# Optimization experiments

Measured on AMD Instinct MI355X. Metric: run time of the kernel, lower is better.

Reference implementation:

```python
import jax, jax.numpy as jnp
import numpy as np

EMBED_DIM = 768
NUM_HEADS = 12
HEAD_DIM = EMBED_DIM // NUM_HEADS
MEMORY_SIZE = 64
B, T = 8, 1024


def setup_inputs() -> dict:
    key = jax.random.key(0)
    ks = jax.random.split(key, 8)
    s = 0.02
    return {
        "x": jax.random.normal(ks[0], (B, T, EMBED_DIM), dtype=jnp.float32),
        "w_qkv": jax.random.normal(ks[1], (EMBED_DIM, 3 * EMBED_DIM), dtype=jnp.float32) * s,
        "b_qkv": jax.random.normal(ks[2], (3 * EMBED_DIM,), dtype=jnp.float32) * s,
        "w_out": jax.random.normal(ks[3], (EMBED_DIM, EMBED_DIM), dtype=jnp.float32) * s,
        "b_out": jax.random.normal(ks[4], (EMBED_DIM,), dtype=jnp.float32) * s,
        "w_mem": jax.random.normal(ks[5], (EMBED_DIM, EMBED_DIM), dtype=jnp.float32) * s,
        "b_mem": jax.random.normal(ks[6], (EMBED_DIM,), dtype=jnp.float32) * s,
        "memory": jax.random.normal(ks[7], (1, MEMORY_SIZE, EMBED_DIM), dtype=jnp.float32),
    }


def reference(x, w_qkv, b_qkv, w_out, b_out, w_mem, b_mem, memory):
    Bx, Tx, C = x.shape
    H, D = NUM_HEADS, HEAD_DIM
    scale = 1.0 / np.sqrt(D).astype(np.float32)

    # qkv projection -> (3, B, H, T, D)
    qkv = (x @ w_qkv + b_qkv).reshape(Bx, Tx, 3, H, D)
    qkv = jnp.transpose(qkv, (2, 0, 3, 1, 4))
    q, k, v = qkv[0], qkv[1], qkv[2]

    # full (non-causal) local attention over T
    scores = jnp.einsum("bhqd,bhkd->bhqk", q, k) * scale  # (B,H,T,T)
    local_out = jnp.einsum("bhqk,bhkd->bhqd", jax.nn.softmax(scores, axis=-1), v)

    # memory attention: projected memory serves as both K and V
    mem = memory @ w_mem + b_mem                      # (1, M, C)
    mem = jnp.broadcast_to(mem, (Bx, MEMORY_SIZE, C))
    mem_kv = jnp.transpose(mem.reshape(Bx, MEMORY_SIZE, H, D), (0, 2, 1, 3))  # (B,H,M,D)
    mem_scores = jnp.einsum("bhqd,bhmd->bhqm", q, mem_kv) * scale
    mem_out = jnp.einsum("bhqm,bhmd->bhqd", jax.nn.softmax(mem_scores, axis=-1), mem_kv)

    out = (local_out + mem_out).transpose(0, 2, 1, 3).reshape(Bx, Tx, C)
    return out @ w_out + b_out
```

## Files before the change

kernel.cpp:

```cpp
#include <hip/hip_runtime.h>

#define EMBED 768
#define NH 12
#define HD 64
#define MEMN 64
#define BB 8
#define TT 1024
#define ROWS 8192
#define QKV_N 2304
#define QSZ 6291456

typedef short bf16x8_t __attribute__((ext_vector_type(8)));
typedef float f32x4_t __attribute__((ext_vector_type(4)));

__device__ __forceinline__ unsigned short f2b(float f){
    union { float f; unsigned int i; } v; v.f = f;
    unsigned int x = v.i;
    unsigned int r = x + 0x7fffu + ((x >> 16) & 1u);
    return (unsigned short)(r >> 16);
}
__device__ __forceinline__ unsigned short f2b_ru(float f){
    union { float f; unsigned int i; } v; v.f = f;
    return (unsigned short)((v.i + 0x8000u) >> 16);
}

__device__ __forceinline__ void gl16(const unsigned short* g, unsigned short* l){
    __builtin_amdgcn_global_load_lds(
        (const __attribute__((address_space(1))) void*)g,
        (__attribute__((address_space(3))) void*)l,
        16, 0, 0);
}

#define SCHED_FENCE() __builtin_amdgcn_sched_barrier(0)

#define PREP_CVT   3072
#define PREP_TQKV  4800
#define PREP_TOUT  5376
#define PREP_TOTAL 5388

__global__ __launch_bounds__(256) void prep_kernel(
    const float* __restrict__ x,
    const float* __restrict__ w_qkv,
    const float* __restrict__ w_out,
    const float* __restrict__ memory,
    const float* __restrict__ w_mem,
    const float* __restrict__ b_mem,
    unsigned short* __restrict__ xb,
    unsigned short* __restrict__ wqkvT,
    unsigned short* __restrict__ woutT,
    unsigned short* __restrict__ mem_k,
    unsigned short* __restrict__ mem_v)
{
    __shared__ unsigned short pool[5120];
    const int bid = blockIdx.x;
    const int t = threadIdx.x;

    if (bid < PREP_CVT) {
        int i = bid * 2048 + t * 8;
        float4 f0 = *(const float4*)&x[i];
        float4 f1 = *(const float4*)&x[i + 4];
        union { bf16x8_t v; unsigned short s[8]; } u;
        u.s[0] = f2b(f0.x); u.s[1] = f2b(f0.y); u.s[2] = f2b(f0.z); u.s[3] = f2b(f0.w);
        u.s[4] = f2b(f1.x); u.s[5] = f2b(f1.y); u.s[6] = f2b(f1.z); u.s[7] = f2b(f1.w);
        *(bf16x8_t*)&xb[i] = u.v;
    } else if (bid < PREP_TOUT) {
        const float* in; unsigned short* out; int R, C, loc;
        if (bid < PREP_TQKV) { in = w_qkv; out = wqkvT; R = EMBED; C = QKV_N; loc = bid - PREP_CVT; }
        else                 { in = w_out; out = woutT; R = EMBED; C = EMBED; loc = bid - PREP_TQKV; }
        int nbc = C / 32;
        int bc = (loc % nbc) * 32, br = (loc / nbc) * 32;
        unsigned short (*tile)[33] = (unsigned short(*)[33])pool;
        int lr = t >> 5, lc = t & 31;
        for (int i = 0; i < 4; i++) {
            int r = lr + i * 8;
            tile[r][lc] = f2b(in[(size_t)(br + r) * C + bc + lc]);
        }
        __syncthreads();
        for (int i = 0; i < 4; i++) {
            int r = lr + i * 8;
            out[(size_t)(bc + r) * R + br + lc] = tile[lc][r];
        }
    } else {
        unsigned short (*As)[40] = (unsigned short(*)[40])pool;
        unsigned short (*Bs)[40] = (unsigned short(*)[40])(pool + 2560);
        int wave = t >> 6, lane = t & 63;
        int ln = lane & 15, lq = lane >> 4;
        int bn = (bid - PREP_TOUT) * 64;
        const int K = EMBED, N = EMBED;

        f32x4_t acc[4];
        for (int i = 0; i < 4; i++) acc[i] = (f32x4_t)(0.f);
        int sm = t >> 2, sk = (t & 3) * 8;
        int bk = t >> 3, bn8 = (t & 7) * 8;

        for (int k0 = 0; k0 < K; k0 += 32) {
            __syncthreads();
            {
                float4 f0 = *(const float4*)&memory[(size_t)sm * K + k0 + sk];
                float4 f1 = *(const float4*)&memory[(size_t)sm * K + k0 + sk + 4];
                unsigned short* ap = &As[sm][sk];
                ap[0] = f2b(f0.x); ap[1] = f2b(f0.y); ap[2] = f2b(f0.z); ap[3] = f2b(f0.w);
                ap[4] = f2b(f1.x); ap[5] = f2b(f1.y); ap[6] = f2b(f1.z); ap[7] = f2b(f1.w);
            }
            {
                float4 g0 = *(const float4*)&w_mem[(size_t)(k0 + bk) * N + bn + bn8];
                float4 g1 = *(const float4*)&w_mem[(size_t)(k0 + bk) * N + bn + bn8 + 4];
                Bs[bn8 + 0][bk] = f2b(g0.x); Bs[bn8 + 1][bk] = f2b(g0.y);
                Bs[bn8 + 2][bk] = f2b(g0.z); Bs[bn8 + 3][bk] = f2b(g0.w);
                Bs[bn8 + 4][bk] = f2b(g1.x); Bs[bn8 + 5][bk] = f2b(g1.y);
                Bs[bn8 + 6][bk] = f2b(g1.z); Bs[bn8 + 7][bk] = f2b(g1.w);
            }
            __syncthreads();
            bf16x8_t a = *(bf16x8_t*)&As[wave * 16 + ln][lq * 8];
            for (int nt = 0; nt < 4; nt++) {
                bf16x8_t bf = *(bf16x8_t*)&Bs[nt * 16 + ln][lq * 8];
                acc[nt] = __builtin_amdgcn_mfma_f32_16x16x32_bf16(a, bf, acc[nt], 0, 0, 0);
            }
        }
        for (int nt = 0; nt < 4; nt++) {
            int c = bn + nt * 16 + ln;
            float bv = b_mem[c];
            for (int r = 0; r < 4; r++) {
                int row = wave * 16 + lq * 4 + r;
                int h = c >> 6, d = c & 63;
                unsigned short o = f2b(acc[nt][r] + bv);
                mem_k[((h * 64 + row) << 6) + d] = o;
                mem_v[((h * 64 + d) << 6) + row] = o;
            }
        }
    }
}

__global__ __launch_bounds__(512) void gemm512(
    const unsigned short* __restrict__ A,
    const unsigned short* __restrict__ BT,
    const float* __restrict__ bias,
    unsigned short* __restrict__ dq,
    unsigned short* __restrict__ dkv,
    int M, int N, int K)
{
    __shared__ unsigned short As[16384];
    __shared__ unsigned short Bs[8192];
    const int t = threadIdx.x;
    const int wave = t >> 6, lane = t & 63;
    const int ln = lane & 15, lq = lane >> 4;
    const int wm = (wave >> 1) * 64, wn = (wave & 1) * 64;

    int bid0 = blockIdx.y * gridDim.x + blockIdx.x;
    int bid = (bid0 & 7) * 72 + (bid0 >> 3);
    int by = bid / 18, bx = bid - by * 18;
    const int bm = by * 256, bn = bx * 128;

    f32x4_t acc[4][4];
    for (int i = 0; i < 4; i++)
        for (int j = 0; j < 4; j++) acc[i][j] = (f32x4_t)(0.f);

    const int rl8 = lane >> 3;
    const int swz = ((lane & 7) ^ rl8) * 8;
    const unsigned short* Ap = A + (size_t)(bm + wave * 32 + rl8) * 768 + swz;
    const unsigned short* Bp = BT + (size_t)(bn + wave * 16 + rl8) * 768 + swz;
    unsigned short* asd = &As[wave * 2048];
    unsigned short* bsd = &Bs[wave * 1024];

    const int e0 = (lq ^ (ln & 7)) * 8;
    const int e1 = e0 ^ 32;

    for (int k0 = 0; k0 < 768; k0 += 64) {
        __syncthreads();
        for (int i = 0; i < 4; i++)
            gl16(Ap + (size_t)(i * 8) * 768 + k0, asd + i * 512);
        for (int i = 0; i < 2; i++)
            gl16(Bp + (size_t)(i * 8) * 768 + k0, bsd + i * 512);
        __syncthreads();

        {
            bf16x8_t af[4], bfr[4];
            for (int mt = 0; mt < 4; mt++)
                af[mt] = *(bf16x8_t*)&As[(wm + mt * 16 + ln) * 64 + e0];
            for (int nt = 0; nt < 4; nt++)
                bfr[nt] = *(bf16x8_t*)&Bs[(wn + nt * 16 + ln) * 64 + e0];
            for (int mt = 0; mt < 4; mt++)
                for (int nt = 0; nt < 4; nt++)
                    acc[mt][nt] = __builtin_amdgcn_mfma_f32_16x16x32_bf16(
                        af[mt], bfr[nt], acc[mt][nt], 0, 0, 0);
        }
        {
            bf16x8_t af[4], bfr[4];
            for (int mt = 0; mt < 4; mt++)
                af[mt] = *(bf16x8_t*)&As[(wm + mt * 16 + ln) * 64 + e1];
            for (int nt = 0; nt < 4; nt++)
                bfr[nt] = *(bf16x8_t*)&Bs[(wn + nt * 16 + ln) * 64 + e1];
            for (int mt = 0; mt < 4; mt++)
                for (int nt = 0; nt < 4; nt++)
                    acc[mt][nt] = __builtin_amdgcn_mfma_f32_16x16x32_bf16(
                        af[mt], bfr[nt], acc[mt][nt], 0, 0, 0);
        }
    }

    __syncthreads();
    unsigned short* slab = &As[wave * 2048];
    const float QSCALE = 0.125f * 1.44269504088896340736f;
    const int s = bn / 768;
    const int rem0 = bn + wn - s * 768;
    const int h = rem0 >> 6;
    const int bbq = bm >> 10;
    const int tt0 = (bm & 1023) + wm;
    const int r2 = lane >> 1, half = lane & 1;

    float bv[4];
    for (int nt = 0; nt < 4; nt++) bv[nt] = bias[bn + wn + nt * 16 + ln];

    for (int p = 0; p < 2; p++) {
        for (int mt2 = 0; mt2 < 2; mt2++) {
            int mt = p * 2 + mt2;
            for (int nt = 0; nt < 4; nt++) {
                int col = nt * 16 + ln;
                for (int r = 0; r < 4; r++) {
                    int tp = mt2 * 16 + lq * 4 + r;
                    float val = acc[mt][nt][r] + bv[nt];
                    if (s == 0) val *= QSCALE;
                    slab[tp * 64 + ((((col >> 3) ^ (tp & 7)) << 3) | (col & 7))] = f2b(val);
                }
            }
        }
        asm volatile("s_waitcnt lgkmcnt(0)" ::: "memory");
        SCHED_FENCE();
        if (s == 0) {
            unsigned short* op = dq + (size_t)(bm + wm + p * 32 + r2) * 768 + bn + wn;
#pragma unroll
            for (int i = 0; i < 4; i++) {
                int c2 = half * 4 + i;
                int g = c2 ^ (r2 & 7);
                *(bf16x8_t*)&op[c2 * 8] = *(bf16x8_t*)&slab[r2 * 64 + g * 8];
            }
        } else if (s == 1) {
            unsigned short* op = dkv +
                (((size_t)(bbq * 12 + h) * 1024 + tt0 + p * 32 + r2) << 6);
#pragma unroll
            for (int i = 0; i < 4; i++) {
                int c2 = half * 4 + i;
                int g = c2 ^ (r2 & 7);
                *(bf16x8_t*)&op[c2 * 8] = *(bf16x8_t*)&slab[r2 * 64 + g * 8];
            }
        } else {
            unsigned short* op0 = dkv + (size_t)QSZ + (((size_t)(bbq * 12 + h)) << 16);
            const int tb = tt0 + p * 32;
#pragma unroll
            for (int i = 0; i < 4; i++) {
                int d = (lane >> 2) + i * 16;
                int t0q = (lane & 3) * 8;
                union { bf16x8_t v; unsigned short s8[8]; } u;
#pragma unroll
                for (int j = 0; j < 8; j++) {
                    int tp = t0q + j;
                    u.s8[j] = slab[tp * 64 + ((((d >> 3) ^ (tp & 7)) << 3) | (d & 7))];
                }
                *(bf16x8_t*)&op0[d * 1024 + tb + t0q] = u.v;
            }
        }
        SCHED_FENCE();
    }
}

__global__ __launch_bounds__(256) void gemm_bt(
    const unsigned short* __restrict__ A,
    const unsigned short* __restrict__ BT,
    const float* __restrict__ bias,
    float* __restrict__ df,
    int M, int N, int K)
{
    __shared__ unsigned short As[2][8192];
    __shared__ unsigned short Bs[2][8192];
    const int t = threadIdx.x;
    const int wave = t >> 6, lane = t & 63;
    const int ln = lane & 15, lq = lane >> 4;
    const int wm = (wave >> 1) * 64, wn = (wave & 1) * 64;
    const int bm = blockIdx.y * 128, bn = blockIdx.x * 128;

    f32x4_t acc[4][4];
    for (int i = 0; i < 4; i++)
        for (int j = 0; j < 4; j++) acc[i][j] = (f32x4_t)(0.f);

    const int rl8 = lane >> 3;
    const int swz = ((lane & 7) ^ rl8) * 8;
    const unsigned short* Ap = A + (size_t)(bm + wave * 32 + rl8) * 768 + swz;
    const unsigned short* Bp = BT + (size_t)(bn + wave * 32 + rl8) * 768 + swz;

    const int e0 = (lq ^ (ln & 7)) * 8;
    const int e1 = e0 ^ 32;

    auto stage = [&](int buf, int k0) {
#pragma unroll
        for (int i = 0; i < 4; i++) {
            gl16(Ap + (size_t)(i * 8) * 768 + k0, &As[buf][wave * 2048 + i * 512]);
            gl16(Bp + (size_t)(i * 8) * 768 + k0, &Bs[buf][wave * 2048 + i * 512]);
        }
    };

    auto compute = [&](const unsigned short* Ac, const unsigned short* Bc) {
        bf16x8_t af0[4], af1[4], bf0[4], bf1[4];
#pragma unroll
        for (int mt = 0; mt < 4; mt++) {
            af0[mt] = *(const bf16x8_t*)&Ac[(wm + mt * 16 + ln) * 64 + e0];
            af1[mt] = *(const bf16x8_t*)&Ac[(wm + mt * 16 + ln) * 64 + e1];
        }
#pragma unroll
        for (int nt = 0; nt < 4; nt++) {
            bf0[nt] = *(const bf16x8_t*)&Bc[(wn + nt * 16 + ln) * 64 + e0];
            bf1[nt] = *(const bf16x8_t*)&Bc[(wn + nt * 16 + ln) * 64 + e1];
        }
        __builtin_amdgcn_s_setprio(1);
#pragma unroll
        for (int mt = 0; mt < 4; mt++)
#pragma unroll
            for (int nt = 0; nt < 4; nt++)
                acc[mt][nt] = __builtin_amdgcn_mfma_f32_16x16x32_bf16(
                    af0[mt], bf0[nt], acc[mt][nt], 0, 0, 0);
#pragma unroll
        for (int mt = 0; mt < 4; mt++)
#pragma unroll
            for (int nt = 0; nt < 4; nt++)
                acc[mt][nt] = __builtin_amdgcn_mfma_f32_16x16x32_bf16(
                    af1[mt], bf1[nt], acc[mt][nt], 0, 0, 0);
        __builtin_amdgcn_s_setprio(0);
    };

    stage(0, 0);
    stage(1, 64);
    SCHED_FENCE();
    asm volatile("s_waitcnt vmcnt(8)" ::: "memory");
    SCHED_FENCE();
    __builtin_amdgcn_s_barrier();
    SCHED_FENCE();

#pragma unroll 2
    for (int tt = 0; tt < 10; ++tt) {
        const int cur = tt & 1;
        compute(&As[cur][0], &Bs[cur][0]);
        SCHED_FENCE();
        __builtin_amdgcn_s_barrier();
        SCHED_FENCE();
        stage(cur, (tt + 2) * 64);
        SCHED_FENCE();
        asm volatile("s_waitcnt vmcnt(8)" ::: "memory");
        SCHED_FENCE();
        __builtin_amdgcn_s_barrier();
        SCHED_FENCE();
    }
    compute(&As[0][0], &Bs[0][0]);
    SCHED_FENCE();
    asm volatile("s_waitcnt vmcnt(0)" ::: "memory");
    SCHED_FENCE();
    __builtin_amdgcn_s_barrier();
    SCHED_FENCE();
    compute(&As[1][0], &Bs[1][0]);

    __syncthreads();
    float* slabf = (float*)&As[0][0] + wave * 2048;
    const int r2 = lane >> 1, half = lane & 1;
    float bv[4];
    for (int nt = 0; nt < 4; nt++) bv[nt] = bias[bn + wn + nt * 16 + ln];

    for (int p = 0; p < 2; p++) {
        for (int mt2 = 0; mt2 < 2; mt2++) {
            int mt = p * 2 + mt2;
            for (int nt = 0; nt < 4; nt++) {
                int col = nt * 16 + ln;
                for (int r = 0; r < 4; r++) {
                    int tp = mt2 * 16 + lq * 4 + r;
                    slabf[tp * 64 + ((((col >> 2) ^ (tp & 15)) << 2) | (col & 3))] =
                        acc[mt][nt][r] + bv[nt];
                }
            }
        }
        asm volatile("s_waitcnt lgkmcnt(0)" ::: "memory");
        SCHED_FENCE();
        float* op = df + (size_t)(bm + wm + p * 32 + r2) * 768 + bn + wn;
#pragma unroll
        for (int i = 0; i < 8; i++) {
            int c2 = half * 8 + i;
            int g = c2 ^ (r2 & 15);
            *(float4*)&op[c2 * 4] = *(float4*)&slabf[r2 * 64 + g * 4];
        }
        SCHED_FENCE();
    }
}

__global__ __launch_bounds__(512) void attn_kernel(
    unsigned short* __restrict__ qio,
    const unsigned short* __restrict__ k_ws,
    const unsigned short* __restrict__ vT_ws,
    const unsigned short* __restrict__ mem_k,
    const unsigned short* __restrict__ mem_v)
{
    __shared__ unsigned short Qs[8192];
    __shared__ unsigned short Ks[8192];
    __shared__ unsigned short Vs[8192];
    unsigned short* Ps = Qs;

    const int t = threadIdx.x;
    const int wave = t >> 6, lane = t & 63;
    const int ln = lane & 15, lq = lane >> 4;
    const int rl = lane >> 3;
    const int cl = ((lane & 7) ^ rl) * 8;

    int bid = blockIdx.x;
    int xcd = bid & 7, rest = bid >> 3;
    int bh = xcd * 12 + (rest >> 3);
    int qt = rest & 7;
    int b = bh / 12, h = bh - b * 12;

    unsigned short* qp = qio + ((size_t)(b * TT + qt * 128)) * 768 + h * 64;
    const unsigned short* kp = k_ws + (size_t)bh * TT * 64;
    const unsigned short* vp = vT_ws + ((size_t)bh << 16);
    const unsigned short* mkp = mem_k + h * 4096;
    const unsigned short* mvp = mem_v + h * 4096;

    {
        const unsigned short* qg = qp + (size_t)(wave * 16 + rl) * 768 + cl;
        gl16(qg, &Qs[wave * 1024]);
        gl16(qg + (size_t)8 * 768, &Qs[wave * 1024 + 512]);
    }
    __syncthreads();
    const int e0 = (lq ^ (ln & 7)) * 8;
    const int e1 = ((lq ^ (ln & 7)) ^ 4) * 8;
    bf16x8_t aq0 = *(bf16x8_t*)&Qs[(wave * 16 + ln) * 64 + e0];
    bf16x8_t aq1 = *(bf16x8_t*)&Qs[(wave * 16 + ln) * 64 + e1];

    const unsigned short* kg = kp + (wave * 16 + rl) * 64 + cl;
    const unsigned short* vg = vp + (size_t)((wave & 3) * 16 + rl) * 1024 + (wave >> 2) * 64 + cl;

    const int hi3 = ln >> 3, lo3 = ln & 7;
    const int pm = (lq & 1) << 2;
    const int pw0 = (wave * 16 + lq * 4) * 64 + lo3;

    float lsum[4] = {0.f, 0.f, 0.f, 0.f};
    f32x4_t accO[4];
    for (int nt = 0; nt < 4; nt++) accO[nt] = (f32x4_t)(0.f);

    for (int kt = 0; kt < 8; kt++) {
        __syncthreads();
        gl16(kg + kt * 8192,        &Ks[wave * 1024]);
        gl16(kg + kt * 8192 + 512,  &Ks[wave * 1024 + 512]);
        gl16(vg + kt * 128,                 &Vs[wave * 1024]);
        gl16(vg + (size_t)8 * 1024 + kt * 128, &Vs[wave * 1024 + 512]);
        __syncthreads();

        for (int half = 0; half < 2; half++) {
            const unsigned short* Kh = &Ks[half * 4096];
            const unsigned short* Vh = &Vs[half * 4096];
            f32x4_t s[4];
            for (int nt = 0; nt < 4; nt++) s[nt] = (f32x4_t)(0.f);
            for (int nt = 0; nt < 4; nt++)
                s[nt] = __builtin_amdgcn_mfma_f32_16x16x32_bf16(
                    aq0, *(bf16x8_t*)&Kh[(nt * 16 + ln) * 64 + e0], s[nt], 0, 0, 0);
            for (int nt = 0; nt < 4; nt++)
                s[nt] = __builtin_amdgcn_mfma_f32_16x16x32_bf16(
                    aq1, *(bf16x8_t*)&Kh[(nt * 16 + ln) * 64 + e1], s[nt], 0, 0, 0);

            for (int nt = 0; nt < 4; nt++) {
                for (int r = 0; r < 4; r++) {
                    float p = __builtin_amdgcn_exp2f(s[nt][r]);
                    lsum[r] += p;
                    int chp = (nt * 2 + hi3) ^ pm ^ r;
                    Ps[pw0 + r * 64 + chp * 8] = f2b_ru(p);
                }
            }
            bf16x8_t a0 = *(bf16x8_t*)&Ps[(wave * 16 + ln) * 64 + e0];
            bf16x8_t a1 = *(bf16x8_t*)&Ps[(wave * 16 + ln) * 64 + e1];
            for (int nt = 0; nt < 4; nt++) {
                accO[nt] = __builtin_amdgcn_mfma_f32_16x16x32_bf16(
                    a0, *(bf16x8_t*)&Vh[(nt * 16 + ln) * 64 + e0], accO[nt], 0, 0, 0);
                accO[nt] = __builtin_amdgcn_mfma_f32_16x16x32_bf16(
                    a1, *(bf16x8_t*)&Vh[(nt * 16 + ln) * 64 + e1], accO[nt], 0, 0, 0);
            }
        }
    }

    __syncthreads();
    gl16(mkp + (wave * 8 + rl) * 64 + cl, &Ks[wave * 512]);
    gl16(mvp + (wave * 8 + rl) * 64 + cl, &Vs[wave * 512]);
    __syncthreads();

    f32x4_t s2[4];
    for (int nt = 0; nt < 4; nt++) s2[nt] = (f32x4_t)(0.f);
    for (int nt = 0; nt < 4; nt++)
        s2[nt] = __builtin_amdgcn_mfma_f32_16x16x32_bf16(
            aq0, *(bf16x8_t*)&Ks[(nt * 16 + ln) * 64 + e0], s2[nt], 0, 0, 0);
    for (int nt = 0; nt < 4; nt++)
        s2[nt] = __builtin_amdgcn_mfma_f32_16x16x32_bf16(
            aq1, *(bf16x8_t*)&Ks[(nt * 16 + ln) * 64 + e1], s2[nt], 0, 0, 0);

    float l2[4] = {0.f, 0.f, 0.f, 0.f};
    for (int nt = 0; nt < 4; nt++) {
        for (int r = 0; r < 4; r++) {
            float p = __builtin_amdgcn_exp2f(s2[nt][r]);
            l2[r] += p;
            int chp = (nt * 2 + hi3) ^ pm ^ r;
            Ps[pw0 + r * 64 + chp * 8] = f2b_ru(p);
        }
    }
    f32x4_t accM[4];
    for (int nt = 0; nt < 4; nt++) accM[nt] = (f32x4_t)(0.f);
    {
        bf16x8_t a0 = *(bf16x8_t*)&Ps[(wave * 16 + ln) * 64 + e0];
        bf16x8_t a1 = *(bf16x8_t*)&Ps[(wave * 16 + ln) * 64 + e1];
        for (int nt = 0; nt < 4; nt++) {
            accM[nt] = __builtin_amdgcn_mfma_f32_16x16x32_bf16(
                a0, *(bf16x8_t*)&Vs[(nt * 16 + ln) * 64 + e0], accM[nt], 0, 0, 0);
            accM[nt] = __builtin_amdgcn_mfma_f32_16x16x32_bf16(
                a1, *(bf16x8_t*)&Vs[(nt * 16 + ln) * 64 + e1], accM[nt], 0, 0, 0);
        }
    }

    float inv[4], inv2[4];
    for (int r = 0; r < 4; r++) {
        float a = lsum[r], c = l2[r];
        a += __shfl_xor(a, 1); a += __shfl_xor(a, 2);
        a += __shfl_xor(a, 4); a += __shfl_xor(a, 8);
        c += __shfl_xor(c, 1); c += __shfl_xor(c, 2);
        c += __shfl_xor(c, 4); c += __shfl_xor(c, 8);
        inv[r] = 1.f / a;
        inv2[r] = 1.f / c;
    }

    for (int nt = 0; nt < 4; nt++) {
        for (int r = 0; r < 4; r++) {
            int lrow = wave * 16 + lq * 4 + r;
            int lcol = nt * 16 + ln;
            float val = accO[nt][r] * inv[r] + accM[nt][r] * inv2[r];
            qp[(size_t)lrow * 768 + lcol] = f2b(val);
        }
    }
}

extern "C" void kernel_launch(void* const* d_in, const int* in_sizes, int n_in,
                              void* d_out, int out_size, void* d_ws, size_t ws_size,
                              hipStream_t stream) {
    const float* x      = (const float*)d_in[0];
    const float* w_qkv  = (const float*)d_in[1];
    const float* b_qkv  = (const float*)d_in[2];
    const float* w_out  = (const float*)d_in[3];
    const float* b_out  = (const float*)d_in[4];
    const float* w_mem  = (const float*)d_in[5];
    const float* b_mem  = (const float*)d_in[6];
    const float* memory = (const float*)d_in[7];

    unsigned short* ws = (unsigned short*)d_ws;
    unsigned short* q_ws   = ws;
    unsigned short* k_ws   = ws + (size_t)QSZ;
    unsigned short* vT     = ws + 2 * (size_t)QSZ;
    unsigned short* woutT  = ws + 3 * (size_t)QSZ;
    unsigned short* mem_k  = woutT + (size_t)EMBED * EMBED;
    unsigned short* mem_v  = mem_k + (size_t)NH * MEMN * HD;

    unsigned short* xb    = (unsigned short*)d_out;
    unsigned short* wqkvT = xb + (size_t)QSZ;

    prep_kernel<<<PREP_TOTAL, 256, 0, stream>>>(
        x, w_qkv, w_out, memory, w_mem, b_mem, xb, wqkvT, woutT, mem_k, mem_v);

    gemm512<<<dim3(QKV_N / 128, ROWS / 256), 512, 0, stream>>>(
        xb, wqkvT, b_qkv, q_ws, k_ws, ROWS, QKV_N, EMBED);

    attn_kernel<<<8 * NH * BB, 512, 0, stream>>>(q_ws, k_ws, vT, mem_k, mem_v);

    gemm_bt<<<dim3(EMBED / 128, ROWS / 128), 256, 0, stream>>>(
        q_ws, woutT, b_out, (float*)d_out, ROWS, EMBED, EMBED);
}
```

Before: 234.0 us.

## Halve attention block to 4 waves, each handling two 16-row query tiles

The attention kernel now runs with 256 threads instead of 512, and each wave processes 32 query rows (two 16-row MFMA tiles) instead of 16. K and V fragments are loaded from LDS once per half-tile and reused across both query tiles, which halves LDS fragment reads per MFMA. The cost is more registers per thread and fewer waves per block to hide latency, with more global-to-LDS loads issued per wave.

```diff
diff --git a/kernel.cpp b/kernel.cpp
--- a/kernel.cpp
+++ b/kernel.cpp
@@ -386,7 +386,7 @@
     }
 }
 
-__global__ __launch_bounds__(512) void attn_kernel(
+__global__ __launch_bounds__(256) void attn_kernel(
     unsigned short* __restrict__ qio,
     const unsigned short* __restrict__ k_ws,
     const unsigned short* __restrict__ vT_ws,
@@ -417,119 +417,194 @@
     const unsigned short* mvp = mem_v + h * 4096;
 
     {
-        const unsigned short* qg = qp + (size_t)(wave * 16 + rl) * 768 + cl;
-        gl16(qg, &Qs[wave * 1024]);
-        gl16(qg + (size_t)8 * 768, &Qs[wave * 1024 + 512]);
+        const unsigned short* qg = qp + (size_t)(wave * 32 + rl) * 768 + cl;
+        gl16(qg,                    &Qs[wave * 2048]);
+        gl16(qg + (size_t) 8 * 768, &Qs[wave * 2048 + 512]);
+        gl16(qg + (size_t)16 * 768, &Qs[wave * 2048 + 1024]);
+        gl16(qg + (size_t)24 * 768, &Qs[wave * 2048 + 1536]);
     }
     __syncthreads();
     const int e0 = (lq ^ (ln & 7)) * 8;
     const int e1 = ((lq ^ (ln & 7)) ^ 4) * 8;
-    bf16x8_t aq0 = *(bf16x8_t*)&Qs[(wave * 16 + ln) * 64 + e0];
-    bf16x8_t aq1 = *(bf16x8_t*)&Qs[(wave * 16 + ln) * 64 + e1];
-
-    const unsigned short* kg = kp + (wave * 16 + rl) * 64 + cl;
-    const unsigned short* vg = vp + (size_t)((wave & 3) * 16 + rl) * 1024 + (wave >> 2) * 64 + cl;
+    bf16x8_t aq[2][2];
+#pragma unroll
+    for (int mt = 0; mt < 2; mt++) {
+        aq[mt][0] = *(bf16x8_t*)&Qs[(wave * 32 + mt * 16 + ln) * 64 + e0];
+        aq[mt][1] = *(bf16x8_t*)&Qs[(wave * 32 + mt * 16 + ln) * 64 + e1];
+    }
+
+    const unsigned short* kg = kp + (size_t)(wave * 32 + rl) * 64 + cl;
+    const unsigned short* vg = vp + (size_t)((wave & 1) * 32 + rl) * 1024 + (wave >> 1) * 64 + cl;
 
     const int hi3 = ln >> 3, lo3 = ln & 7;
     const int pm = (lq & 1) << 2;
-    const int pw0 = (wave * 16 + lq * 4) * 64 + lo3;
-
-    float lsum[4] = {0.f, 0.f, 0.f, 0.f};
-    f32x4_t accO[4];
-    for (int nt = 0; nt < 4; nt++) accO[nt] = (f32x4_t)(0.f);
+    const int pw0 = (wave * 32 + lq * 4) * 64 + lo3;
+
+    float lsum[2][4];
+#pragma unroll
+    for (int mt = 0; mt < 2; mt++)
+        for (int r = 0; r < 4; r++) lsum[mt][r] = 0.f;
+    f32x4_t accO[2][4];
+#pragma unroll
+    for (int mt = 0; mt < 2; mt++)
+        for (int nt = 0; nt < 4; nt++) accO[mt][nt] = (f32x4_t)(0.f);
 
     for (int kt = 0; kt < 8; kt++) {
         __syncthreads();
-        gl16(kg + kt * 8192,        &Ks[wave * 1024]);
-        gl16(kg + kt * 8192 + 512,  &Ks[wave * 1024 + 512]);
-        gl16(vg + kt * 128,                 &Vs[wave * 1024]);
-        gl16(vg + (size_t)8 * 1024 + kt * 128, &Vs[wave * 1024 + 512]);
+#pragma unroll
+        for (int i = 0; i < 4; i++) {
+            gl16(kg + kt * 8192 + i * 512,          &Ks[wave * 2048 + i * 512]);
+            gl16(vg + kt * 128 + (size_t)i * 8192,  &Vs[wave * 2048 + i * 512]);
+        }
         __syncthreads();
 
         for (int half = 0; half < 2; half++) {
             const unsigned short* Kh = &Ks[half * 4096];
             const unsigned short* Vh = &Vs[half * 4096];
-            f32x4_t s[4];
-            for (int nt = 0; nt < 4; nt++) s[nt] = (f32x4_t)(0.f);
+            bf16x8_t kf0[4], kf1[4];
+#pragma unroll
+            for (int nt = 0; nt < 4; nt++) {
+                kf0[nt] = *(bf16x8_t*)&Kh[(nt * 16 + ln) * 64 + e0];
+                kf1[nt] = *(bf16x8_t*)&Kh[(nt * 16 + ln) * 64 + e1];
+            }
+#pragma unroll
+            for (int mt = 0; mt < 2; mt++) {
+                f32x4_t s[4];
+#pragma unroll
+                for (int nt = 0; nt < 4; nt++) s[nt] = (f32x4_t)(0.f);
+#pragma unroll
+                for (int nt = 0; nt < 4; nt++)
+                    s[nt] = __builtin_amdgcn_mfma_f32_16x16x32_bf16(
+                        aq[mt][0], kf0[nt], s[nt], 0, 0, 0);
+#pragma unroll
+                for (int nt = 0; nt < 4; nt++)
+                    s[nt] = __builtin_amdgcn_mfma_f32_16x16x32_bf16(
+                        aq[mt][1], kf1[nt], s[nt], 0, 0, 0);
+#pragma unroll
+                for (int nt = 0; nt < 4; nt++) {
+#pragma unroll
+                    for (int r = 0; r < 4; r++) {
+                        float p = __builtin_amdgcn_exp2f(s[nt][r]);
+                        lsum[mt][r] += p;
+                        int chp = (nt * 2 + hi3) ^ pm ^ r;
+                        Ps[pw0 + mt * 1024 + r * 64 + chp * 8] = f2b_ru(p);
+                    }
+                }
+            }
+            bf16x8_t vf0[4], vf1[4];
+#pragma unroll
+            for (int nt = 0; nt < 4; nt++) {
+                vf0[nt] = *(bf16x8_t*)&Vh[(nt * 16 + ln) * 64 + e0];
+                vf1[nt] = *(bf16x8_t*)&Vh[(nt * 16 + ln) * 64 + e1];
+            }
+#pragma unroll
+            for (int mt = 0; mt < 2; mt++) {
+                bf16x8_t a0 = *(bf16x8_t*)&Ps[(wave * 32 + mt * 16 + ln) * 64 + e0];
+                bf16x8_t a1 = *(bf16x8_t*)&Ps[(wave * 32 + mt * 16 + ln) * 64 + e1];
+#pragma unroll
+                for (int nt = 0; nt < 4; nt++) {
+                    accO[mt][nt] = __builtin_amdgcn_mfma_f32_16x16x32_bf16(
+                        a0, vf0[nt], accO[mt][nt], 0, 0, 0);
+                    accO[mt][nt] = __builtin_amdgcn_mfma_f32_16x16x32_bf16(
+                        a1, vf1[nt], accO[mt][nt], 0, 0, 0);
+                }
+            }
+        }
+    }
+
+    __syncthreads();
+    gl16(mkp + (size_t)(wave * 16 + rl) * 64 + cl,     &Ks[wave * 1024]);
+    gl16(mkp + (size_t)(wave * 16 + 8 + rl) * 64 + cl, &Ks[wave * 1024 + 512]);
+    gl16(mvp + (size_t)(wave * 16 + rl) * 64 + cl,     &Vs[wave * 1024]);
+    gl16(mvp + (size_t)(wave * 16 + 8 + rl) * 64 + cl, &Vs[wave * 1024 + 512]);
+    __syncthreads();
+
+    float l2[2][4];
+#pragma unroll
+    for (int mt = 0; mt < 2; mt++)
+        for (int r = 0; r < 4; r++) l2[mt][r] = 0.f;
+    f32x4_t accM[2][4];
+#pragma unroll
+    for (int mt = 0; mt < 2; mt++)
+        for (int nt = 0; nt < 4; nt++) accM[mt][nt] = (f32x4_t)(0.f);
+
+    {
+        bf16x8_t kf0[4], kf1[4];
+#pragma unroll
+        for (int nt = 0; nt < 4; nt++) {
+            kf0[nt] = *(bf16x8_t*)&Ks[(nt * 16 + ln) * 64 + e0];
+            kf1[nt] = *(bf16x8_t*)&Ks[(nt * 16 + ln) * 64 + e1];
+        }
+#pragma unroll
+        for (int mt = 0; mt < 2; mt++) {
+            f32x4_t s2[4];
+#pragma unroll
+            for (int nt = 0; nt < 4; nt++) s2[nt] = (f32x4_t)(0.f);
+#pragma unroll
             for (int nt = 0; nt < 4; nt++)
-                s[nt] = __builtin_amdgcn_mfma_f32_16x16x32_bf16(
-                    aq0, *(bf16x8_t*)&Kh[(nt * 16 + ln) * 64 + e0], s[nt], 0, 0, 0);
+                s2[nt] = __builtin_amdgcn_mfma_f32_16x16x32_bf16(
+                    aq[mt][0], kf0[nt], s2[nt], 0, 0, 0);
+#pragma unroll
             for (int nt = 0; nt < 4; nt++)
-                s[nt] = __builtin_amdgcn_mfma_f32_16x16x32_bf16(
-                    aq1, *(bf16x8_t*)&Kh[(nt * 16 + ln) * 64 + e1], s[nt], 0, 0, 0);
-
+                s2[nt] = __builtin_amdgcn_mfma_f32_16x16x32_bf16(
+                    aq[mt][1], kf1[nt], s2[nt], 0, 0, 0);
+#pragma unroll
             for (int nt = 0; nt < 4; nt++) {
+#pragma unroll
                 for (int r = 0; r < 4; r++) {
-                    float p = __builtin_amdgcn_exp2f(s[nt][r]);
-                    lsum[r] += p;
+                    float p = __builtin_amdgcn_exp2f(s2[nt][r]);
+                    l2[mt][r] += p;
                     int chp = (nt * 2 + hi3) ^ pm ^ r;
-                    Ps[pw0 + r * 64 + chp * 8] = f2b_ru(p);
+                    Ps[pw0 + mt * 1024 + r * 64 + chp * 8] = f2b_ru(p);
                 }
             }
-            bf16x8_t a0 = *(bf16x8_t*)&Ps[(wave * 16 + ln) * 64 + e0];
-            bf16x8_t a1 = *(bf16x8_t*)&Ps[(wave * 16 + ln) * 64 + e1];
+        }
+        bf16x8_t vf0[4], vf1[4];
+#pragma unroll
+        for (int nt = 0; nt < 4; nt++) {
+            vf0[nt] = *(bf16x8_t*)&Vs[(nt * 16 + ln) * 64 + e0];
+            vf1[nt] = *(bf16x8_t*)&Vs[(nt * 16 + ln) * 64 + e1];
+        }
+#pragma unroll
+        for (int mt = 0; mt < 2; mt++) {
+            bf16x8_t a0 = *(bf16x8_t*)&Ps[(wave * 32 + mt * 16 + ln) * 64 + e0];
+            bf16x8_t a1 = *(bf16x8_t*)&Ps[(wave * 32 + mt * 16 + ln) * 64 + e1];
+#pragma unroll
             for (int nt = 0; nt < 4; nt++) {
-                accO[nt] = __builtin_amdgcn_mfma_f32_16x16x32_bf16(
-                    a0, *(bf16x8_t*)&Vh[(nt * 16 + ln) * 64 + e0], accO[nt], 0, 0, 0);
-                accO[nt] = __builtin_amdgcn_mfma_f32_16x16x32_bf16(
-                    a1, *(bf16x8_t*)&Vh[(nt * 16 + ln) * 64 + e1], accO[nt], 0, 0, 0);
-            }
-        }
-    }
-
-    __syncthreads();
-    gl16(mkp + (wave * 8 + rl) * 64 + cl, &Ks[wave * 512]);
-    gl16(mvp + (wave * 8 + rl) * 64 + cl, &Vs[wave * 512]);
-    __syncthreads();
-
-    f32x4_t s2[4];
-    for (int nt = 0; nt < 4; nt++) s2[nt] = (f32x4_t)(0.f);
-    for (int nt = 0; nt < 4; nt++)
-        s2[nt] = __builtin_amdgcn_mfma_f32_16x16x32_bf16(
-            aq0, *(bf16x8_t*)&Ks[(nt * 16 + ln) * 64 + e0], s2[nt], 0, 0, 0);
-    for (int nt = 0; nt < 4; nt++)
-        s2[nt] = __builtin_amdgcn_mfma_f32_16x16x32_bf16(
-            aq1, *(bf16x8_t*)&Ks[(nt * 16 + ln) * 64 + e1], s2[nt], 0, 0, 0);
-
-    float l2[4] = {0.f, 0.f, 0.f, 0.f};
-    for (int nt = 0; nt < 4; nt++) {
+                accM[mt][nt] = __builtin_amdgcn_mfma_f32_16x16x32_bf16(
+                    a0, vf0[nt], accM[mt][nt], 0, 0, 0);
+                accM[mt][nt] = __builtin_amdgcn_mfma_f32_16x16x32_bf16(
+                    a1, vf1[nt], accM[mt][nt], 0, 0, 0);
+            }
+        }
+    }
+
+    float inv[2][4], inv2[2][4];
+#pragma unroll
+    for (int mt = 0; mt < 2; mt++) {
+#pragma unroll
         for (int r = 0; r < 4; r++) {
-            float p = __builtin_amdgcn_exp2f(s2[nt][r]);
-            l2[r] += p;
-            int chp = (nt * 2 + hi3) ^ pm ^ r;
-            Ps[pw0 + r * 64 + chp * 8] = f2b_ru(p);
-        }
-    }
-    f32x4_t accM[4];
-    for (int nt = 0; nt < 4; nt++) accM[nt] = (f32x4_t)(0.f);
-    {
-        bf16x8_t a0 = *(bf16x8_t*)&Ps[(wave * 16 + ln) * 64 + e0];
-        bf16x8_t a1 = *(bf16x8_t*)&Ps[(wave * 16 + ln) * 64 + e1];
+            float a = lsum[mt][r], c = l2[mt][r];
+            a += __shfl_xor(a, 1); a += __shfl_xor(a, 2);
+            a += __shfl_xor(a, 4); a += __shfl_xor(a, 8);
+            c += __shfl_xor(c, 1); c += __shfl_xor(c, 2);
+            c += __shfl_xor(c, 4); c += __shfl_xor(c, 8);
+            inv[mt][r] = 1.f / a;
+            inv2[mt][r] = 1.f / c;
+        }
+    }
+
+#pragma unroll
+    for (int mt = 0; mt < 2; mt++) {
+#pragma unroll
         for (int nt = 0; nt < 4; nt++) {
-            accM[nt] = __builtin_amdgcn_mfma_f32_16x16x32_bf16(
-                a0, *(bf16x8_t*)&Vs[(nt * 16 + ln) * 64 + e0], accM[nt], 0, 0, 0);
-            accM[nt] = __builtin_amdgcn_mfma_f32_16x16x32_bf16(
-                a1, *(bf16x8_t*)&Vs[(nt * 16 + ln) * 64 + e1], accM[nt], 0, 0, 0);
-        }
-    }
-
-    float inv[4], inv2[4];
-    for (int r = 0; r < 4; r++) {
-        float a = lsum[r], c = l2[r];
-        a += __shfl_xor(a, 1); a += __shfl_xor(a, 2);
-        a += __shfl_xor(a, 4); a += __shfl_xor(a, 8);
-        c += __shfl_xor(c, 1); c += __shfl_xor(c, 2);
-        c += __shfl_xor(c, 4); c += __shfl_xor(c, 8);
-        inv[r] = 1.f / a;
-        inv2[r] = 1.f / c;
-    }
-
-    for (int nt = 0; nt < 4; nt++) {
-        for (int r = 0; r < 4; r++) {
-            int lrow = wave * 16 + lq * 4 + r;
-            int lcol = nt * 16 + ln;
-            float val = accO[nt][r] * inv[r] + accM[nt][r] * inv2[r];
-            qp[(size_t)lrow * 768 + lcol] = f2b(val);
+#pragma unroll
+            for (int r = 0; r < 4; r++) {
+                int lrow = wave * 32 + mt * 16 + lq * 4 + r;
+                int lcol = nt * 16 + ln;
+                float val = accO[mt][nt][r] * inv[mt][r] + accM[mt][nt][r] * inv2[mt][r];
+                qp[(size_t)lrow * 768 + lcol] = f2b(val);
+            }
         }
     }
 }
@@ -563,7 +638,7 @@
     gemm512<<<dim3(QKV_N / 128, ROWS / 256), 512, 0, stream>>>(
         xb, wqkvT, b_qkv, q_ws, k_ws, ROWS, QKV_N, EMBED);
 
-    attn_kernel<<<8 * NH * BB, 512, 0, stream>>>(q_ws, k_ws, vT, mem_k, mem_v);
+    attn_kernel<<<8 * NH * BB, 256, 0, stream>>>(q_ws, k_ws, vT, mem_k, mem_v);
 
     gemm_bt<<<dim3(EMBED / 128, ROWS / 128), 256, 0, stream>>>(
         q_ws, woutT, b_out, (float*)d_out, ROWS, EMBED, EMBED);
```

Result: no change. 236.6 us (+1.1%).
